# Kernel tuning notes

Measured on AMD Instinct MI355X. Metric: run time of the kernel, lower is better.

## Reference

```python
import jax, jax.numpy as jnp
import numpy as np

D_MODEL = 256
D_INNER = 512   # expand=2
D_STATE = 16
DT_RANK = 16    # ceil(d_model/16)
D_CONV = 4
N_LAYERS = 2    # per direction
B, N = 2, 1024


def _mamba_layer(x, W_in, cw, cb, W_x, W_dt, b_dt, A_log, Dp, W_out):
    """One mamba_ssm.Mamba forward. x: (B, L, d_model)."""
    Bb, L, _ = x.shape
    xz = x @ W_in.T                        # (B, L, 2*d_inner)
    di = xz.shape[-1] // 2
    xc, z = xz[..., :di], xz[..., di:]
    # causal depthwise conv1d, kernel D_CONV, left-pad d_conv-1
    K = cw.shape[-1]
    xp = jnp.pad(xc, ((0, 0), (K - 1, 0), (0, 0)))
    xc = sum(xp[:, k:k + L, :] * cw[:, k] for k in range(K)) + cb
    xc = jax.nn.silu(xc)
    # input-dependent dt, B, C
    dbl = xc @ W_x.T                       # (B, L, dt_rank + 2*d_state)
    ds = A_log.shape[-1]
    dt = dbl[..., :DT_RANK]
    Bm = dbl[..., DT_RANK:DT_RANK + ds]    # (B, L, d_state)
    Cm = dbl[..., DT_RANK + ds:]           # (B, L, d_state)
    dt = jax.nn.softplus(dt @ W_dt.T + b_dt)  # (B, L, d_inner)
    A = -jnp.exp(A_log)                    # (d_inner, d_state)
    dA = jnp.exp(dt[..., None] * A)                          # (B, L, di, ds)
    dBx = dt[..., None] * Bm[:, :, None, :] * xc[..., None]  # (B, L, di, ds)

    def step(h, inp):
        a_t, b_t, c_t = inp                # (B,di,ds),(B,di,ds),(B,ds)
        h = a_t * h + b_t
        y_t = jnp.einsum('bds,bs->bd', h, c_t)
        return h, y_t

    h0 = jnp.zeros((Bb, di, ds), x.dtype)
    _, ys = jax.lax.scan(step, h0, (dA.transpose(1, 0, 2, 3),
                                    dBx.transpose(1, 0, 2, 3),
                                    Cm.transpose(1, 0, 2)))
    y = ys.transpose(1, 0, 2) + xc * Dp    # skip term D*x
    y = y * jax.nn.silu(z)                 # gate
    return y @ W_out.T                     # (B, L, d_model)


def setup_inputs() -> dict:
    key = jax.random.key(0)
    ks = jax.random.split(key, 10)
    s = 0.05  # weight scale for numerical stability
    nlay = 2 * N_LAYERS  # forward layers then backward layers
    return {
        "x": jax.random.normal(ks[0], (B, N, D_MODEL), jnp.float32),
        "in_proj": jax.random.normal(ks[1], (nlay, 2 * D_INNER, D_MODEL), jnp.float32) * s,
        "conv_w": jax.random.normal(ks[2], (nlay, D_INNER, D_CONV), jnp.float32) * s,
        "conv_b": jax.random.normal(ks[3], (nlay, D_INNER), jnp.float32) * s,
        "x_proj": jax.random.normal(ks[4], (nlay, DT_RANK + 2 * D_STATE, D_INNER), jnp.float32) * s,
        "dt_proj": jax.random.normal(ks[5], (nlay, D_INNER, DT_RANK), jnp.float32) * s,
        "dt_bias": jax.random.normal(ks[6], (nlay, D_INNER), jnp.float32) * s,
        "A_log": jax.random.uniform(ks[7], (nlay, D_INNER, D_STATE), jnp.float32),
        "D": jax.random.uniform(ks[8], (nlay, D_INNER), jnp.float32),
        "out_proj": jax.random.normal(ks[9], (nlay, D_MODEL, D_INNER), jnp.float32) * s,
    }


def reference(x, in_proj, conv_w, conv_b, x_proj, dt_proj, dt_bias, A_log, D, out_proj):
    n = in_proj.shape[0] // 2
    x_fwd = x
    for i in range(n):
        x_fwd = _mamba_layer(x_fwd, in_proj[i], conv_w[i], conv_b[i], x_proj[i],
                             dt_proj[i], dt_bias[i], A_log[i], D[i], out_proj[i])
    x_bwd = x[:, ::-1, :]
    for i in range(n, 2 * n):
        x_bwd = _mamba_layer(x_bwd, in_proj[i], conv_w[i], conv_b[i], x_proj[i],
                             dt_proj[i], dt_bias[i], A_log[i], D[i], out_proj[i])
    x_bwd = x_bwd[:, ::-1, :]
    return jnp.concatenate([x_fwd, x_bwd], axis=-1)  # (B, N, 2*d_model)
```

## Files before the change

### kernel.cpp

```cpp
#include <hip/hip_runtime.h>
#include <math.h>

#define G 2
#define BB 2
#define L 1024
#define DM 256
#define DI 512
#define DS 16
#define DR 16
#define CH 64
#define CL 16
#define RTOT (G*BB*L)
#define SKX 8

typedef short bh8 __attribute__((ext_vector_type(8)));
typedef float f4x __attribute__((ext_vector_type(4)));

__device__ __forceinline__ float silu_f(float x) { return x / (1.f + __expf(-x)); }

__device__ __forceinline__ unsigned short f2bf(float f) {
    unsigned u = __float_as_uint(f);
    unsigned r = u + 0x7FFFu + ((u >> 16) & 1u);
    return (unsigned short)(r >> 16);
}
__device__ __forceinline__ float bf2f(unsigned short s) {
    return __uint_as_float(((unsigned)s) << 16);
}

template<int BM, int SPLITK, int AMAP, int CMODE>
__global__ __launch_bounds__(256) void mfma_gemm(
    const float* __restrict__ A, size_t slabOff, int lda, int Ktot,
    const float* __restrict__ W, int Nout, int step,
    float* __restrict__ C, int ldc, size_t partStride)
{
    constexpr int AP = BM / 32;
    constexpr int CA = BM / 32;
    __shared__ short As_hi[BM * 40];
    __shared__ short As_lo[BM * 40];
    __shared__ short Bs_hi[64 * 40];
    __shared__ short Bs_lo[64 * 40];

    const int row0 = blockIdx.y * BM;
    const int col0 = blockIdx.x * 64;
    const int g    = row0 >> 11;
    const int lay  = g * 2 + step;
    const float* Wg = W + (size_t)lay * Nout * Ktot;
    const int t    = threadIdx.x;
    const int lane = t & 63, wv = t >> 6;
    const int m = lane & 15, quad = lane >> 4;
    const int wr = wv >> 1, wc = wv & 1;

    const int Kc    = Ktot / SPLITK;
    const int kbase = blockIdx.z * Kc;
    const int NT    = Kc / 32;

    float4 pa[CA], pa2[CA], pb[2];
    auto loadT = [&](int kt) {
        const int kb = kbase + kt * 32;
        #pragma unroll
        for (int i = 0; i < CA; i++) {
            int id = t + 256 * i;
            int row = id >> 3, kq = id & 7;
            size_t arow;
            if (AMAP == 1) {
                int gr = row0 + row;
                int gg = gr >> 11, b = (gr >> 10) & 1, l = gr & 1023;
                int sl = gg ? (1023 - l) : l;
                arow = (size_t)(b * 1024 + sl);
            } else {
                arow = (size_t)(row0 + row);
            }
            pa[i] = *(const float4*)&A[arow * lda + kb + kq * 4];
            if (AMAP == 2)
                pa2[i] = *(const float4*)&A[slabOff + arow * lda + kb + kq * 4];
        }
        #pragma unroll
        for (int i = 0; i < 2; i++) {
            int id = t + 256 * i;
            int row = id >> 3, kq = id & 7;
            pb[i] = *(const float4*)&Wg[(size_t)(col0 + row) * Ktot + kb + kq * 4];
        }
    };
    auto cvt_store = [&](short* hi, short* lo, int row, int kq, float4 v) {
        short4 h, l;
        unsigned short s;
        s = f2bf(v.x); h.x = (short)s; l.x = (short)f2bf(v.x - bf2f(s));
        s = f2bf(v.y); h.y = (short)s; l.y = (short)f2bf(v.y - bf2f(s));
        s = f2bf(v.z); h.z = (short)s; l.z = (short)f2bf(v.z - bf2f(s));
        s = f2bf(v.w); h.w = (short)s; l.w = (short)f2bf(v.w - bf2f(s));
        *(short4*)&hi[row * 40 + kq * 4] = h;
        *(short4*)&lo[row * 40 + kq * 4] = l;
    };

    f4x acc[AP][2] = {};
    loadT(0);

    for (int kt = 0; kt < NT; kt++) {
        #pragma unroll
        for (int i = 0; i < CA; i++) {
            int id = t + 256 * i;
            int row = id >> 3, kq = id & 7;
            float4 v = pa[i];
            if (AMAP == 2) { v.x += pa2[i].x; v.y += pa2[i].y; v.z += pa2[i].z; v.w += pa2[i].w; }
            cvt_store(As_hi, As_lo, row, kq, v);
        }
        #pragma unroll
        for (int i = 0; i < 2; i++) {
            int id = t + 256 * i;
            int row = id >> 3, kq = id & 7;
            cvt_store(Bs_hi, Bs_lo, row, kq, pb[i]);
        }
        __syncthreads();
        if (kt + 1 < NT) loadT(kt + 1);

        bh8 ah[AP], al[AP], bh[2], bl[2];
        #pragma unroll
        for (int p = 0; p < AP; p++) {
            int r = wr * (BM / 2) + p * 16 + m;
            ah[p] = *(bh8*)&As_hi[r * 40 + quad * 8];
            al[p] = *(bh8*)&As_lo[r * 40 + quad * 8];
        }
        #pragma unroll
        for (int pb_ = 0; pb_ < 2; pb_++) {
            int r = wc * 32 + pb_ * 16 + m;
            bh[pb_] = *(bh8*)&Bs_hi[r * 40 + quad * 8];
            bl[pb_] = *(bh8*)&Bs_lo[r * 40 + quad * 8];
        }
        #pragma unroll
        for (int p = 0; p < AP; p++)
            #pragma unroll
            for (int q = 0; q < 2; q++) {
                acc[p][q] = __builtin_amdgcn_mfma_f32_16x16x32_bf16(ah[p], bh[q], acc[p][q], 0, 0, 0);
                acc[p][q] = __builtin_amdgcn_mfma_f32_16x16x32_bf16(ah[p], bl[q], acc[p][q], 0, 0, 0);
                acc[p][q] = __builtin_amdgcn_mfma_f32_16x16x32_bf16(al[p], bh[q], acc[p][q], 0, 0, 0);
            }
        __syncthreads();
    }

    float* Cz = C + (size_t)blockIdx.z * partStride;
    #pragma unroll
    for (int p = 0; p < AP; p++)
        #pragma unroll
        for (int q = 0; q < 2; q++) {
            int gcol = col0 + wc * 32 + q * 16 + m;
            #pragma unroll
            for (int r = 0; r < 4; r++) {
                int grow = row0 + wr * (BM / 2) + p * 16 + quad * 4 + r;
                if (CMODE == 2) {
                    int b = (grow >> 10) & 1, l = grow & 1023;
                    size_t dst = (g == 0)
                        ? ((size_t)(b * 1024 + l) * 512 + gcol)
                        : ((size_t)(b * 1024 + (1023 - l)) * 512 + 256 + gcol);
                    C[dst] = acc[p][q][r];
                } else {
                    Cz[(size_t)grow * ldc + gcol] = acc[p][q][r];
                }
            }
        }
}

template<int SPLITK>
__global__ __launch_bounds__(256) void gemm_xproj(
    const float* __restrict__ XZ, const float* __restrict__ cw,
    const float* __restrict__ cb, float* __restrict__ XCb,
    const float* __restrict__ W, int step,
    float* __restrict__ C, size_t partStride)
{
    constexpr int Nout = 48, Ktot = DI;
    __shared__ float As[16][68];
    __shared__ float Bs[16][68];

    const int row0 = blockIdx.y * 64;
    const int g    = row0 >> 11;
    const int lay  = g * 2 + step;
    const float* Wg = W + (size_t)lay * Nout * Ktot;
    const int t  = threadIdx.x;
    const int tx = t & 15, ty = t >> 4;
    const int Kc    = Ktot / SPLITK;
    const int kbase = blockIdx.z * Kc;
    const int NT    = Kc / 16;

    const int sr = t >> 2;
    const int sk = (t & 3) * 4;
    const int gr = row0 + sr;
    const int l  = gr & 1023;
    const bool bok = (sr < Nout);

    float4 pa, pb;
    auto loadT = [&](int kt) {
        const int ch = kbase + kt * 16 + sk;
        const float* wb = cw + ((size_t)lay * 512 + ch) * 4;
        float4 w0 = *(const float4*)&wb[0];
        float4 w1 = *(const float4*)&wb[4];
        float4 w2 = *(const float4*)&wb[8];
        float4 w3 = *(const float4*)&wb[12];
        float4 acc = *(const float4*)&cb[(size_t)lay * 512 + ch];
        #pragma unroll
        for (int k = 0; k < 4; k++) {
            if (l - 3 + k < 0) continue;
            float4 xv = *(const float4*)&XZ[(size_t)(gr - 3 + k) * 1024 + ch];
            acc.x += (&w0.x)[k] * xv.x; acc.y += (&w1.x)[k] * xv.y;
            acc.z += (&w2.x)[k] * xv.z; acc.w += (&w3.x)[k] * xv.w;
        }
        acc.x = silu_f(acc.x); acc.y = silu_f(acc.y);
        acc.z = silu_f(acc.z); acc.w = silu_f(acc.w);
        pa = acc;
        *(float4*)&XCb[(size_t)gr * 512 + ch] = acc;
        pb = bok ? *(const float4*)&Wg[(size_t)sr * Ktot + kbase + kt * 16 + sk]
                 : make_float4(0.f, 0.f, 0.f, 0.f);
    };

    float acc[4][4] = {};
    loadT(0);

    for (int kt = 0; kt < NT; kt++) {
        As[sk + 0][sr] = pa.x; As[sk + 1][sr] = pa.y;
        As[sk + 2][sr] = pa.z; As[sk + 3][sr] = pa.w;
        Bs[sk + 0][sr] = pb.x; Bs[sk + 1][sr] = pb.y;
        Bs[sk + 2][sr] = pb.z; Bs[sk + 3][sr] = pb.w;
        __syncthreads();
        if (kt + 1 < NT) loadT(kt + 1);
        #pragma unroll
        for (int kk = 0; kk < 16; kk++) {
            float4 a = *(const float4*)&As[kk][ty * 4];
            float4 b = *(const float4*)&Bs[kk][tx * 4];
            float av[4] = {a.x, a.y, a.z, a.w};
            float bv[4] = {b.x, b.y, b.z, b.w};
            #pragma unroll
            for (int i = 0; i < 4; i++)
                #pragma unroll
                for (int j = 0; j < 4; j++) acc[i][j] += av[i] * bv[j];
        }
        __syncthreads();
    }

    float* Cz = C + (size_t)blockIdx.z * partStride;
    const int col = tx * 4;
    if (col < Nout) {
        #pragma unroll
        for (int i = 0; i < 4; i++) {
            int r = row0 + ty * 4 + i;
            *(float4*)&Cz[(size_t)r * 48 + col] =
                make_float4(acc[i][0], acc[i][1], acc[i][2], acc[i][3]);
        }
    }
}

__device__ __forceinline__ void stage_dbl(
    float dbl[CL][48], const float* __restrict__ Pdbl, int r0, int tid)
{
    for (int id = tid; id < CL * 48; id += 512) {
        int rr = id / 48, cc = id - rr * 48;
        size_t o = (size_t)(r0 + rr) * 48 + cc;
        float v = 0.f;
        #pragma unroll
        for (int s = 0; s < SKX; s++) v += Pdbl[(size_t)s * (RTOT * 48) + o];
        dbl[rr][cc] = v;
    }
}

__global__ __launch_bounds__(512) void scanA(
    const float* __restrict__ XCb, const float* __restrict__ Pdbl,
    const float* __restrict__ A_log, const float* __restrict__ Wdt,
    const float* __restrict__ bdt,
    float* __restrict__ Aprod, float* __restrict__ Hend, int step)
{
    __shared__ float dbl[CL][48];
    int blk = blockIdx.x;
    int c  = blk & (CH - 1);
    int gb = blk >> 6;
    int g  = gb >> 1;
    int lay = g * 2 + step;
    int d = threadIdx.x;
    int r0 = gb * L + c * CL;

    stage_dbl(dbl, Pdbl, r0, threadIdx.x);

    float wdt[16];
    const float* wrow = Wdt + ((size_t)lay * DI + d) * DR;
    #pragma unroll
    for (int k = 0; k < 16; k += 4) {
        float4 v = *(const float4*)&wrow[k];
        wdt[k] = v.x; wdt[k + 1] = v.y; wdt[k + 2] = v.z; wdt[k + 3] = v.w;
    }
    float bias = bdt[(size_t)lay * DI + d];

    float a[DS], h[DS], ap[DS];
    const float* al = A_log + ((size_t)lay * DI + d) * DS;
    #pragma unroll
    for (int s = 0; s < DS; s++) { a[s] = -__expf(al[s]); h[s] = 0.f; ap[s] = 1.f; }
    __syncthreads();

    for (int tt = 0; tt < CL; tt++) {
        float dtr = bias;
        #pragma unroll
        for (int k = 0; k < 16; k++) dtr += dbl[tt][k] * wdt[k];
        float dt = (dtr > 20.f) ? dtr : log1pf(__expf(dtr));
        float xc = XCb[(size_t)(r0 + tt) * DI + d];
        float dx = dt * xc;
        #pragma unroll
        for (int s = 0; s < DS; s++) {
            float da = __expf(dt * a[s]);
            h[s] = da * h[s] + dx * dbl[tt][16 + s];
            ap[s] *= da;
        }
    }
    size_t base = ((size_t)(gb * DI + d) * CH + c) * DS;
    #pragma unroll
    for (int q = 0; q < 4; q++) {
        *(float4*)&Aprod[base + q * 4] = make_float4(ap[q*4], ap[q*4+1], ap[q*4+2], ap[q*4+3]);
        *(float4*)&Hend [base + q * 4] = make_float4(h[q*4],  h[q*4+1],  h[q*4+2],  h[q*4+3]);
    }
}

__global__ __launch_bounds__(256) void scanCombine(
    const float* __restrict__ Aprod, const float* __restrict__ Hend,
    float* __restrict__ Hinit)
{
    int idx = blockIdx.x * 256 + threadIdx.x;
    int s  = idx & 15;
    int gd = idx >> 4;
    size_t base = (size_t)gd * CH * DS + s;
    float h = 0.f;
    for (int c0 = 0; c0 < CH; c0 += 8) {
        float ap[8], e[8];
        #pragma unroll
        for (int j = 0; j < 8; j++) {
            size_t o = base + (size_t)(c0 + j) * DS;
            ap[j] = Aprod[o]; e[j] = Hend[o];
        }
        #pragma unroll
        for (int j = 0; j < 8; j++) {
            Hinit[base + (size_t)(c0 + j) * DS] = h;
            h = ap[j] * h + e[j];
        }
    }
}

__global__ __launch_bounds__(512) void scanB(
    const float* __restrict__ XCb, const float* __restrict__ Pdbl,
    const float* __restrict__ XZ, const float* __restrict__ A_log,
    const float* __restrict__ Wdt, const float* __restrict__ bdt,
    const float* __restrict__ Dp, const float* __restrict__ Hinit,
    float* __restrict__ Yb, int step)
{
    __shared__ float dbl[CL][48];
    int blk = blockIdx.x;
    int c  = blk & (CH - 1);
    int gb = blk >> 6;
    int g  = gb >> 1;
    int lay = g * 2 + step;
    int d = threadIdx.x;
    int r0 = gb * L + c * CL;

    stage_dbl(dbl, Pdbl, r0, threadIdx.x);

    float wdt[16];
    const float* wrow = Wdt + ((size_t)lay * DI + d) * DR;
    #pragma unroll
    for (int k = 0; k < 16; k += 4) {
        float4 v = *(const float4*)&wrow[k];
        wdt[k] = v.x; wdt[k + 1] = v.y; wdt[k + 2] = v.z; wdt[k + 3] = v.w;
    }
    float bias = bdt[(size_t)lay * DI + d];

    float a[DS], h[DS];
    const float* al = A_log + ((size_t)lay * DI + d) * DS;
    size_t base = ((size_t)(gb * DI + d) * CH + c) * DS;
    #pragma unroll
    for (int s = 0; s < DS; s++) { a[s] = -__expf(al[s]); h[s] = Hinit[base + s]; }
    float Dv = Dp[(size_t)lay * DI + d];
    __syncthreads();

    for (int tt = 0; tt < CL; tt++) {
        int r = r0 + tt;
        float dtr = bias;
        #pragma unroll
        for (int k = 0; k < 16; k++) dtr += dbl[tt][k] * wdt[k];
        float dt = (dtr > 20.f) ? dtr : log1pf(__expf(dtr));
        float xc = XCb[(size_t)r * DI + d];
        float dx = dt * xc;
        float y = 0.f;
        #pragma unroll
        for (int s = 0; s < DS; s++) {
            float da = __expf(dt * a[s]);
            h[s] = da * h[s] + dx * dbl[tt][16 + s];
            y += h[s] * dbl[tt][32 + s];
        }
        y += xc * Dv;
        float z = XZ[(size_t)r * 1024 + 512 + d];
        y *= silu_f(z);
        Yb[(size_t)r * DI + d] = y;
    }
}

extern "C" void kernel_launch(void* const* d_in, const int* in_sizes, int n_in,
                              void* d_out, int out_size, void* d_ws, size_t ws_size,
                              hipStream_t stream)
{
    const float* x        = (const float*)d_in[0];
    const float* in_proj  = (const float*)d_in[1];
    const float* conv_w   = (const float*)d_in[2];
    const float* conv_b   = (const float*)d_in[3];
    const float* x_proj   = (const float*)d_in[4];
    const float* dt_proj  = (const float*)d_in[5];
    const float* dt_bias  = (const float*)d_in[6];
    const float* A_log    = (const float*)d_in[7];
    const float* Dp       = (const float*)d_in[8];
    const float* out_proj = (const float*)d_in[9];
    float* out = (float*)d_out;

    float* w = (float*)d_ws;
    size_t o = 0;
    float* XZ    = w + o; o += (size_t)RTOT * 1024;
    float* XCb   = w + o; o += (size_t)RTOT * DI;
    float* Yb    = w + o; o += (size_t)RTOT * DI;
    float* Pdbl  = w + o; o += (size_t)SKX * RTOT * 48;
    float* Aprod = w + o; o += (size_t)G * BB * DI * CH * DS;
    float* Hend  = w + o; o += (size_t)G * BB * DI * CH * DS;
    float* Hinit = w + o; o += (size_t)G * BB * DI * CH * DS;
    float* Pout  = w + o; o += (size_t)2 * RTOT * DM;
    (void)ws_size; (void)in_sizes; (void)n_in; (void)out_size;

    for (int step = 0; step < 2; step++) {
        if (step == 0)
            mfma_gemm<128, 1, 1, 0><<<dim3(16, 32, 1), 256, 0, stream>>>(
                x, 0, DM, DM, in_proj, 2 * DI, 0, XZ, 1024, 0);
        else
            mfma_gemm<128, 1, 2, 0><<<dim3(16, 32, 1), 256, 0, stream>>>(
                Pout, (size_t)RTOT * DM, DM, DM, in_proj, 2 * DI, 1, XZ, 1024, 0);

        gemm_xproj<SKX><<<dim3(1, 64, SKX), 256, 0, stream>>>(
            XZ, conv_w, conv_b, XCb, x_proj, step, Pdbl, (size_t)RTOT * 48);

        scanA<<<G * BB * CH, 512, 0, stream>>>(
            XCb, Pdbl, A_log, dt_proj, dt_bias, Aprod, Hend, step);
        scanCombine<<<(G * BB * DI * DS) / 256, 256, 0, stream>>>(Aprod, Hend, Hinit);
        scanB<<<G * BB * CH, 512, 0, stream>>>(
            XCb, Pdbl, XZ, A_log, dt_proj, dt_bias, Dp, Hinit, Yb, step);

        if (step == 0)
            mfma_gemm<64, 2, 0, 0><<<dim3(4, 64, 2), 256, 0, stream>>>(
                Yb, 0, DI, DI, out_proj, DM, 0, Pout, DM, (size_t)RTOT * DM);
        else
            mfma_gemm<64, 1, 0, 2><<<dim3(4, 64, 1), 256, 0, stream>>>(
                Yb, 0, DI, DI, out_proj, DM, 1, out, DM, 0);
    }
}
```

Measured before the change: 266.3 us.

## Use split-bf16 MFMA for x_proj and cache dt/dbl between scan passes

The fused conv+x_proj GEMM moves from a scalar FP32 outer-product loop to bf16 MFMA with a hi/lo split (three MFMAs per tile) to keep near-FP32 accuracy. scanA now writes the reduced split-K dbl rows and the softplus dt values to workspace. scanB reads these instead of re-reducing the split-K partials and recomputing the dt projection. Both scans preload xc, z and dt into register arrays and fully unroll the time loop, at the cost of extra global traffic for the DTb buffer and more register pressure.

```diff
diff --git a/kernel.cpp b/kernel.cpp
--- a/kernel.cpp
+++ b/kernel.cpp
@@ -160,109 +160,142 @@
 }
 
 template<int SPLITK>
-__global__ __launch_bounds__(256) void gemm_xproj(
+__global__ __launch_bounds__(256) void mfma_xproj(
     const float* __restrict__ XZ, const float* __restrict__ cw,
     const float* __restrict__ cb, float* __restrict__ XCb,
     const float* __restrict__ W, int step,
     float* __restrict__ C, size_t partStride)
 {
     constexpr int Nout = 48, Ktot = DI;
-    __shared__ float As[16][68];
-    __shared__ float Bs[16][68];
+    __shared__ short As_hi[64 * 40];
+    __shared__ short As_lo[64 * 40];
+    __shared__ short Bs_hi[64 * 40];
+    __shared__ short Bs_lo[64 * 40];
 
     const int row0 = blockIdx.y * 64;
     const int g    = row0 >> 11;
     const int lay  = g * 2 + step;
     const float* Wg = W + (size_t)lay * Nout * Ktot;
-    const int t  = threadIdx.x;
-    const int tx = t & 15, ty = t >> 4;
+    const int t    = threadIdx.x;
+    const int lane = t & 63, wv = t >> 6;
+    const int m = lane & 15, quad = lane >> 4;
+    const int wr = wv >> 1, wc = wv & 1;
+
     const int Kc    = Ktot / SPLITK;
     const int kbase = blockIdx.z * Kc;
-    const int NT    = Kc / 16;
-
-    const int sr = t >> 2;
-    const int sk = (t & 3) * 4;
-    const int gr = row0 + sr;
-    const int l  = gr & 1023;
-    const bool bok = (sr < Nout);
-
-    float4 pa, pb;
+    const int NT    = Kc / 32;
+
+    float4 pa[2], pb[2];
     auto loadT = [&](int kt) {
-        const int ch = kbase + kt * 16 + sk;
-        const float* wb = cw + ((size_t)lay * 512 + ch) * 4;
-        float4 w0 = *(const float4*)&wb[0];
-        float4 w1 = *(const float4*)&wb[4];
-        float4 w2 = *(const float4*)&wb[8];
-        float4 w3 = *(const float4*)&wb[12];
-        float4 acc = *(const float4*)&cb[(size_t)lay * 512 + ch];
-        #pragma unroll
-        for (int k = 0; k < 4; k++) {
-            if (l - 3 + k < 0) continue;
-            float4 xv = *(const float4*)&XZ[(size_t)(gr - 3 + k) * 1024 + ch];
-            acc.x += (&w0.x)[k] * xv.x; acc.y += (&w1.x)[k] * xv.y;
-            acc.z += (&w2.x)[k] * xv.z; acc.w += (&w3.x)[k] * xv.w;
-        }
-        acc.x = silu_f(acc.x); acc.y = silu_f(acc.y);
-        acc.z = silu_f(acc.z); acc.w = silu_f(acc.w);
-        pa = acc;
-        *(float4*)&XCb[(size_t)gr * 512 + ch] = acc;
-        pb = bok ? *(const float4*)&Wg[(size_t)sr * Ktot + kbase + kt * 16 + sk]
-                 : make_float4(0.f, 0.f, 0.f, 0.f);
+        const int kb = kbase + kt * 32;
+        #pragma unroll
+        for (int i = 0; i < 2; i++) {
+            int id = t + 256 * i;
+            int row = id >> 3, kq = id & 7;
+            int gr = row0 + row;
+            int l  = gr & 1023;
+            int ch = kb + kq * 4;
+            const float* wb = cw + ((size_t)lay * 512 + ch) * 4;
+            float4 w0 = *(const float4*)&wb[0];
+            float4 w1 = *(const float4*)&wb[4];
+            float4 w2 = *(const float4*)&wb[8];
+            float4 w3 = *(const float4*)&wb[12];
+            float4 acc = *(const float4*)&cb[(size_t)lay * 512 + ch];
+            #pragma unroll
+            for (int k = 0; k < 4; k++) {
+                if (l - 3 + k < 0) continue;
+                float4 xv = *(const float4*)&XZ[(size_t)(gr - 3 + k) * 1024 + ch];
+                acc.x += (&w0.x)[k] * xv.x; acc.y += (&w1.x)[k] * xv.y;
+                acc.z += (&w2.x)[k] * xv.z; acc.w += (&w3.x)[k] * xv.w;
+            }
+            acc.x = silu_f(acc.x); acc.y = silu_f(acc.y);
+            acc.z = silu_f(acc.z); acc.w = silu_f(acc.w);
+            pa[i] = acc;
+            *(float4*)&XCb[(size_t)gr * 512 + ch] = acc;
+        }
+        #pragma unroll
+        for (int i = 0; i < 2; i++) {
+            int id = t + 256 * i;
+            int row = id >> 3, kq = id & 7;
+            pb[i] = (row < Nout)
+                  ? *(const float4*)&Wg[(size_t)row * Ktot + kb + kq * 4]
+                  : make_float4(0.f, 0.f, 0.f, 0.f);
+        }
     };
-
-    float acc[4][4] = {};
+    auto cvt_store = [&](short* hi, short* lo, int row, int kq, float4 v) {
+        short4 h, l;
+        unsigned short s;
+        s = f2bf(v.x); h.x = (short)s; l.x = (short)f2bf(v.x - bf2f(s));
+        s = f2bf(v.y); h.y = (short)s; l.y = (short)f2bf(v.y - bf2f(s));
+        s = f2bf(v.z); h.z = (short)s; l.z = (short)f2bf(v.z - bf2f(s));
+        s = f2bf(v.w); h.w = (short)s; l.w = (short)f2bf(v.w - bf2f(s));
+        *(short4*)&hi[row * 40 + kq * 4] = h;
+        *(short4*)&lo[row * 40 + kq * 4] = l;
+    };
+
+    f4x acc[2][2] = {};
     loadT(0);
 
     for (int kt = 0; kt < NT; kt++) {
-        As[sk + 0][sr] = pa.x; As[sk + 1][sr] = pa.y;
-        As[sk + 2][sr] = pa.z; As[sk + 3][sr] = pa.w;
-        Bs[sk + 0][sr] = pb.x; Bs[sk + 1][sr] = pb.y;
-        Bs[sk + 2][sr] = pb.z; Bs[sk + 3][sr] = pb.w;
+        #pragma unroll
+        for (int i = 0; i < 2; i++) {
+            int id = t + 256 * i;
+            int row = id >> 3, kq = id & 7;
+            cvt_store(As_hi, As_lo, row, kq, pa[i]);
+        }
+        #pragma unroll
+        for (int i = 0; i < 2; i++) {
+            int id = t + 256 * i;
+            int row = id >> 3, kq = id & 7;
+            cvt_store(Bs_hi, Bs_lo, row, kq, pb[i]);
+        }
         __syncthreads();
         if (kt + 1 < NT) loadT(kt + 1);
-        #pragma unroll
-        for (int kk = 0; kk < 16; kk++) {
-            float4 a = *(const float4*)&As[kk][ty * 4];
-            float4 b = *(const float4*)&Bs[kk][tx * 4];
-            float av[4] = {a.x, a.y, a.z, a.w};
-            float bv[4] = {b.x, b.y, b.z, b.w};
+
+        bh8 ah[2], al[2], bh[2], bl[2];
+        #pragma unroll
+        for (int p = 0; p < 2; p++) {
+            int r = wr * 32 + p * 16 + m;
+            ah[p] = *(bh8*)&As_hi[r * 40 + quad * 8];
+            al[p] = *(bh8*)&As_lo[r * 40 + quad * 8];
+        }
+        #pragma unroll
+        for (int q = 0; q < 2; q++) {
+            int r = wc * 32 + q * 16 + m;
+            bh[q] = *(bh8*)&Bs_hi[r * 40 + quad * 8];
+            bl[q] = *(bh8*)&Bs_lo[r * 40 + quad * 8];
+        }
+        #pragma unroll
+        for (int p = 0; p < 2; p++)
             #pragma unroll
-            for (int i = 0; i < 4; i++)
-                #pragma unroll
-                for (int j = 0; j < 4; j++) acc[i][j] += av[i] * bv[j];
-        }
+            for (int q = 0; q < 2; q++) {
+                acc[p][q] = __builtin_amdgcn_mfma_f32_16x16x32_bf16(ah[p], bh[q], acc[p][q], 0, 0, 0);
+                acc[p][q] = __builtin_amdgcn_mfma_f32_16x16x32_bf16(ah[p], bl[q], acc[p][q], 0, 0, 0);
+                acc[p][q] = __builtin_amdgcn_mfma_f32_16x16x32_bf16(al[p], bh[q], acc[p][q], 0, 0, 0);
+            }
         __syncthreads();
     }
 
     float* Cz = C + (size_t)blockIdx.z * partStride;
-    const int col = tx * 4;
-    if (col < Nout) {
-        #pragma unroll
-        for (int i = 0; i < 4; i++) {
-            int r = row0 + ty * 4 + i;
-            *(float4*)&Cz[(size_t)r * 48 + col] =
-                make_float4(acc[i][0], acc[i][1], acc[i][2], acc[i][3]);
-        }
-    }
-}
-
-__device__ __forceinline__ void stage_dbl(
-    float dbl[CL][48], const float* __restrict__ Pdbl, int r0, int tid)
-{
-    for (int id = tid; id < CL * 48; id += 512) {
-        int rr = id / 48, cc = id - rr * 48;
-        size_t o = (size_t)(r0 + rr) * 48 + cc;
-        float v = 0.f;
-        #pragma unroll
-        for (int s = 0; s < SKX; s++) v += Pdbl[(size_t)s * (RTOT * 48) + o];
-        dbl[rr][cc] = v;
-    }
+    #pragma unroll
+    for (int p = 0; p < 2; p++)
+        #pragma unroll
+        for (int q = 0; q < 2; q++) {
+            int gcol = wc * 32 + q * 16 + m;
+            if (gcol >= Nout) continue;
+            #pragma unroll
+            for (int r = 0; r < 4; r++) {
+                int grow = row0 + wr * 32 + p * 16 + quad * 4 + r;
+                Cz[(size_t)grow * 48 + gcol] = acc[p][q][r];
+            }
+        }
 }
 
 __global__ __launch_bounds__(512) void scanA(
     const float* __restrict__ XCb, const float* __restrict__ Pdbl,
     const float* __restrict__ A_log, const float* __restrict__ Wdt,
     const float* __restrict__ bdt,
+    float* __restrict__ DBLc, float* __restrict__ DTb,
     float* __restrict__ Aprod, float* __restrict__ Hend, int step)
 {
     __shared__ float dbl[CL][48];
@@ -274,7 +307,15 @@
     int d = threadIdx.x;
     int r0 = gb * L + c * CL;
 
-    stage_dbl(dbl, Pdbl, r0, threadIdx.x);
+    for (int id = threadIdx.x; id < CL * 48; id += 512) {
+        int rr = id / 48, cc = id - rr * 48;
+        size_t o = (size_t)(r0 + rr) * 48 + cc;
+        float v = 0.f;
+        #pragma unroll
+        for (int s = 0; s < SKX; s++) v += Pdbl[(size_t)s * (RTOT * 48) + o];
+        dbl[rr][cc] = v;
+        DBLc[o] = v;
+    }
 
     float wdt[16];
     const float* wrow = Wdt + ((size_t)lay * DI + d) * DR;
@@ -285,19 +326,24 @@
     }
     float bias = bdt[(size_t)lay * DI + d];
 
+    float xc[CL];
+    #pragma unroll
+    for (int tt = 0; tt < CL; tt++) xc[tt] = XCb[(size_t)(r0 + tt) * DI + d];
+
     float a[DS], h[DS], ap[DS];
     const float* al = A_log + ((size_t)lay * DI + d) * DS;
     #pragma unroll
     for (int s = 0; s < DS; s++) { a[s] = -__expf(al[s]); h[s] = 0.f; ap[s] = 1.f; }
     __syncthreads();
 
+    #pragma unroll
     for (int tt = 0; tt < CL; tt++) {
         float dtr = bias;
         #pragma unroll
         for (int k = 0; k < 16; k++) dtr += dbl[tt][k] * wdt[k];
         float dt = (dtr > 20.f) ? dtr : log1pf(__expf(dtr));
-        float xc = XCb[(size_t)(r0 + tt) * DI + d];
-        float dx = dt * xc;
+        DTb[(size_t)(r0 + tt) * DI + d] = dt;
+        float dx = dt * xc[tt];
         #pragma unroll
         for (int s = 0; s < DS; s++) {
             float da = __expf(dt * a[s]);
@@ -338,11 +384,10 @@
 }
 
 __global__ __launch_bounds__(512) void scanB(
-    const float* __restrict__ XCb, const float* __restrict__ Pdbl,
+    const float* __restrict__ XCb, const float* __restrict__ DBLc,
     const float* __restrict__ XZ, const float* __restrict__ A_log,
-    const float* __restrict__ Wdt, const float* __restrict__ bdt,
-    const float* __restrict__ Dp, const float* __restrict__ Hinit,
-    float* __restrict__ Yb, int step)
+    const float* __restrict__ DTb, const float* __restrict__ Dp,
+    const float* __restrict__ Hinit, float* __restrict__ Yb, int step)
 {
     __shared__ float dbl[CL][48];
     int blk = blockIdx.x;
@@ -353,16 +398,18 @@
     int d = threadIdx.x;
     int r0 = gb * L + c * CL;
 
-    stage_dbl(dbl, Pdbl, r0, threadIdx.x);
-
-    float wdt[16];
-    const float* wrow = Wdt + ((size_t)lay * DI + d) * DR;
-    #pragma unroll
-    for (int k = 0; k < 16; k += 4) {
-        float4 v = *(const float4*)&wrow[k];
-        wdt[k] = v.x; wdt[k + 1] = v.y; wdt[k + 2] = v.z; wdt[k + 3] = v.w;
-    }
-    float bias = bdt[(size_t)lay * DI + d];
+    for (int id = threadIdx.x; id < CL * 48; id += 512) {
+        int rr = id / 48, cc = id - rr * 48;
+        dbl[rr][cc] = DBLc[(size_t)(r0 + rr) * 48 + cc];
+    }
+
+    float xc[CL], zz[CL], dt[CL];
+    #pragma unroll
+    for (int tt = 0; tt < CL; tt++) xc[tt] = XCb[(size_t)(r0 + tt) * DI + d];
+    #pragma unroll
+    for (int tt = 0; tt < CL; tt++) zz[tt] = XZ[(size_t)(r0 + tt) * 1024 + 512 + d];
+    #pragma unroll
+    for (int tt = 0; tt < CL; tt++) dt[tt] = DTb[(size_t)(r0 + tt) * DI + d];
 
     float a[DS], h[DS];
     const float* al = A_log + ((size_t)lay * DI + d) * DS;
@@ -372,25 +419,19 @@
     float Dv = Dp[(size_t)lay * DI + d];
     __syncthreads();
 
+    #pragma unroll
     for (int tt = 0; tt < CL; tt++) {
-        int r = r0 + tt;
-        float dtr = bias;
-        #pragma unroll
-        for (int k = 0; k < 16; k++) dtr += dbl[tt][k] * wdt[k];
-        float dt = (dtr > 20.f) ? dtr : log1pf(__expf(dtr));
-        float xc = XCb[(size_t)r * DI + d];
-        float dx = dt * xc;
+        float dx = dt[tt] * xc[tt];
         float y = 0.f;
         #pragma unroll
         for (int s = 0; s < DS; s++) {
-            float da = __expf(dt * a[s]);
+            float da = __expf(dt[tt] * a[s]);
             h[s] = da * h[s] + dx * dbl[tt][16 + s];
             y += h[s] * dbl[tt][32 + s];
         }
-        y += xc * Dv;
-        float z = XZ[(size_t)r * 1024 + 512 + d];
-        y *= silu_f(z);
-        Yb[(size_t)r * DI + d] = y;
+        y += xc[tt] * Dv;
+        y *= silu_f(zz[tt]);
+        Yb[(size_t)(r0 + tt) * DI + d] = y;
     }
 }
 
@@ -416,6 +457,8 @@
     float* XCb   = w + o; o += (size_t)RTOT * DI;
     float* Yb    = w + o; o += (size_t)RTOT * DI;
     float* Pdbl  = w + o; o += (size_t)SKX * RTOT * 48;
+    float* DBLc  = w + o; o += (size_t)RTOT * 48;
+    float* DTb   = w + o; o += (size_t)RTOT * DI;
     float* Aprod = w + o; o += (size_t)G * BB * DI * CH * DS;
     float* Hend  = w + o; o += (size_t)G * BB * DI * CH * DS;
     float* Hinit = w + o; o += (size_t)G * BB * DI * CH * DS;
@@ -430,14 +473,14 @@
             mfma_gemm<128, 1, 2, 0><<<dim3(16, 32, 1), 256, 0, stream>>>(
                 Pout, (size_t)RTOT * DM, DM, DM, in_proj, 2 * DI, 1, XZ, 1024, 0);
 
-        gemm_xproj<SKX><<<dim3(1, 64, SKX), 256, 0, stream>>>(
+        mfma_xproj<SKX><<<dim3(1, 64, SKX), 256, 0, stream>>>(
             XZ, conv_w, conv_b, XCb, x_proj, step, Pdbl, (size_t)RTOT * 48);
 
         scanA<<<G * BB * CH, 512, 0, stream>>>(
-            XCb, Pdbl, A_log, dt_proj, dt_bias, Aprod, Hend, step);
+            XCb, Pdbl, A_log, dt_proj, dt_bias, DBLc, DTb, Aprod, Hend, step);
         scanCombine<<<(G * BB * DI * DS) / 256, 256, 0, stream>>>(Aprod, Hend, Hinit);
         scanB<<<G * BB * CH, 512, 0, stream>>>(
-            XCb, Pdbl, XZ, A_log, dt_proj, dt_bias, Dp, Hinit, Yb, step);
+            XCb, DBLc, XZ, A_log, DTb, Dp, Hinit, Yb, step);
 
         if (step == 0)
             mfma_gemm<64, 2, 0, 0><<<dim3(4, 64, 2), 256, 0, stream>>>(
```

New measurement: 280.0 us. 1.05x slower.

## Fuse out_proj GEMM into scan phase-B kernel via LDS-staged bf16x3 MFMA

Applied to the files above, without the earlier changes.

The scanB kernel now keeps its gated output for a 16-row chunk in shared memory as hi/lo bf16 pairs, then multiplies it by out_proj with MFMA and writes the projected result straight to Pout or to the final output. This drops the Yb intermediate, the separate out_proj GEMM launch and the split-K partial buffer, so the next in_proj no longer sums two slabs. In exchange, each of the 256 blocks reloads and converts the whole 256x512 out_proj weight from global memory with no reuse across blocks, and the M tile is only 16 rows, which adds a lot of redundant weight traffic and conversion ALU work.

```diff
diff --git a/kernel.cpp b/kernel.cpp
--- a/kernel.cpp
+++ b/kernel.cpp
@@ -12,6 +12,7 @@
 #define CL 16
 #define RTOT (G*BB*L)
 #define SKX 8
+#define YSTR 520
 
 typedef short bh8 __attribute__((ext_vector_type(8)));
 typedef float f4x __attribute__((ext_vector_type(4)));
@@ -27,9 +28,9 @@
     return __uint_as_float(((unsigned)s) << 16);
 }
 
-template<int BM, int SPLITK, int AMAP, int CMODE>
+template<int BM, int SPLITK, int AMAP>
 __global__ __launch_bounds__(256) void mfma_gemm(
-    const float* __restrict__ A, size_t slabOff, int lda, int Ktot,
+    const float* __restrict__ A, int lda, int Ktot,
     const float* __restrict__ W, int Nout, int step,
     float* __restrict__ C, int ldc, size_t partStride)
 {
@@ -54,7 +55,7 @@
     const int kbase = blockIdx.z * Kc;
     const int NT    = Kc / 32;
 
-    float4 pa[CA], pa2[CA], pb[2];
+    float4 pa[CA], pb[2];
     auto loadT = [&](int kt) {
         const int kb = kbase + kt * 32;
         #pragma unroll
@@ -71,8 +72,6 @@
                 arow = (size_t)(row0 + row);
             }
             pa[i] = *(const float4*)&A[arow * lda + kb + kq * 4];
-            if (AMAP == 2)
-                pa2[i] = *(const float4*)&A[slabOff + arow * lda + kb + kq * 4];
         }
         #pragma unroll
         for (int i = 0; i < 2; i++) {
@@ -100,9 +99,7 @@
         for (int i = 0; i < CA; i++) {
             int id = t + 256 * i;
             int row = id >> 3, kq = id & 7;
-            float4 v = pa[i];
-            if (AMAP == 2) { v.x += pa2[i].x; v.y += pa2[i].y; v.z += pa2[i].z; v.w += pa2[i].w; }
-            cvt_store(As_hi, As_lo, row, kq, v);
+            cvt_store(As_hi, As_lo, row, kq, pa[i]);
         }
         #pragma unroll
         for (int i = 0; i < 2; i++) {
@@ -146,15 +143,7 @@
             #pragma unroll
             for (int r = 0; r < 4; r++) {
                 int grow = row0 + wr * (BM / 2) + p * 16 + quad * 4 + r;
-                if (CMODE == 2) {
-                    int b = (grow >> 10) & 1, l = grow & 1023;
-                    size_t dst = (g == 0)
-                        ? ((size_t)(b * 1024 + l) * 512 + gcol)
-                        : ((size_t)(b * 1024 + (1023 - l)) * 512 + 256 + gcol);
-                    C[dst] = acc[p][q][r];
-                } else {
-                    Cz[(size_t)grow * ldc + gcol] = acc[p][q][r];
-                }
+                Cz[(size_t)grow * ldc + gcol] = acc[p][q][r];
             }
         }
 }
@@ -337,14 +326,17 @@
     }
 }
 
-__global__ __launch_bounds__(512) void scanB(
+template<int OUTMODE>
+__global__ __launch_bounds__(512) void scanB_fused(
     const float* __restrict__ XCb, const float* __restrict__ Pdbl,
     const float* __restrict__ XZ, const float* __restrict__ A_log,
     const float* __restrict__ Wdt, const float* __restrict__ bdt,
     const float* __restrict__ Dp, const float* __restrict__ Hinit,
-    float* __restrict__ Yb, int step)
+    const float* __restrict__ Wout, float* __restrict__ Cout, int step)
 {
     __shared__ float dbl[CL][48];
+    __shared__ short Ys_hi[CL * YSTR];
+    __shared__ short Ys_lo[CL * YSTR];
     int blk = blockIdx.x;
     int c  = blk & (CH - 1);
     int gb = blk >> 6;
@@ -390,7 +382,56 @@
         y += xc * Dv;
         float z = XZ[(size_t)r * 1024 + 512 + d];
         y *= silu_f(z);
-        Yb[(size_t)r * DI + d] = y;
+        unsigned short hs = f2bf(y);
+        Ys_hi[tt * YSTR + d] = (short)hs;
+        Ys_lo[tt * YSTR + d] = (short)f2bf(y - bf2f(hs));
+    }
+    __syncthreads();
+
+    const int lane = threadIdx.x & 63, wv = threadIdx.x >> 6;
+    const int m = lane & 15, quad = lane >> 4;
+    const float* Wg2 = Wout + (size_t)lay * DM * DI;
+
+    #pragma unroll
+    for (int q = 0; q < 2; q++) {
+        const int coln = wv * 32 + q * 16 + m;
+        const float* wp = Wg2 + (size_t)coln * DI;
+        f4x acc = {};
+        #pragma unroll
+        for (int k0 = 0; k0 < DI; k0 += 32) {
+            const int kk = k0 + quad * 8;
+            float4 w0 = *(const float4*)&wp[kk];
+            float4 w1 = *(const float4*)&wp[kk + 4];
+            bh8 bhv, blv;
+            {
+                float vv[8] = {w0.x, w0.y, w0.z, w0.w, w1.x, w1.y, w1.z, w1.w};
+                #pragma unroll
+                for (int j = 0; j < 8; j++) {
+                    unsigned short hsj = f2bf(vv[j]);
+                    bhv[j] = (short)hsj;
+                    blv[j] = (short)f2bf(vv[j] - bf2f(hsj));
+                }
+            }
+            bh8 ahv = *(bh8*)&Ys_hi[m * YSTR + kk];
+            bh8 alv = *(bh8*)&Ys_lo[m * YSTR + kk];
+            acc = __builtin_amdgcn_mfma_f32_16x16x32_bf16(ahv, bhv, acc, 0, 0, 0);
+            acc = __builtin_amdgcn_mfma_f32_16x16x32_bf16(ahv, blv, acc, 0, 0, 0);
+            acc = __builtin_amdgcn_mfma_f32_16x16x32_bf16(alv, bhv, acc, 0, 0, 0);
+        }
+        #pragma unroll
+        for (int r = 0; r < 4; r++) {
+            int tt = quad * 4 + r;
+            int grow = r0 + tt;
+            if (OUTMODE == 0) {
+                Cout[(size_t)grow * DM + coln] = acc[r];
+            } else {
+                int b = (grow >> 10) & 1, l = grow & 1023;
+                size_t dst = (g == 0)
+                    ? ((size_t)(b * 1024 + l) * 512 + coln)
+                    : ((size_t)(b * 1024 + (1023 - l)) * 512 + 256 + coln);
+                Cout[dst] = acc[r];
+            }
+        }
     }
 }
 
@@ -414,21 +455,20 @@
     size_t o = 0;
     float* XZ    = w + o; o += (size_t)RTOT * 1024;
     float* XCb   = w + o; o += (size_t)RTOT * DI;
-    float* Yb    = w + o; o += (size_t)RTOT * DI;
     float* Pdbl  = w + o; o += (size_t)SKX * RTOT * 48;
     float* Aprod = w + o; o += (size_t)G * BB * DI * CH * DS;
     float* Hend  = w + o; o += (size_t)G * BB * DI * CH * DS;
     float* Hinit = w + o; o += (size_t)G * BB * DI * CH * DS;
-    float* Pout  = w + o; o += (size_t)2 * RTOT * DM;
+    float* Pout  = w + o; o += (size_t)RTOT * DM;
     (void)ws_size; (void)in_sizes; (void)n_in; (void)out_size;
 
     for (int step = 0; step < 2; step++) {
         if (step == 0)
-            mfma_gemm<128, 1, 1, 0><<<dim3(16, 32, 1), 256, 0, stream>>>(
-                x, 0, DM, DM, in_proj, 2 * DI, 0, XZ, 1024, 0);
+            mfma_gemm<128, 1, 1><<<dim3(16, 32, 1), 256, 0, stream>>>(
+                x, DM, DM, in_proj, 2 * DI, 0, XZ, 1024, 0);
         else
-            mfma_gemm<128, 1, 2, 0><<<dim3(16, 32, 1), 256, 0, stream>>>(
-                Pout, (size_t)RTOT * DM, DM, DM, in_proj, 2 * DI, 1, XZ, 1024, 0);
+            mfma_gemm<128, 1, 0><<<dim3(16, 32, 1), 256, 0, stream>>>(
+                Pout, DM, DM, in_proj, 2 * DI, 1, XZ, 1024, 0);
 
         gemm_xproj<SKX><<<dim3(1, 64, SKX), 256, 0, stream>>>(
             XZ, conv_w, conv_b, XCb, x_proj, step, Pdbl, (size_t)RTOT * 48);
@@ -436,14 +476,13 @@
         scanA<<<G * BB * CH, 512, 0, stream>>>(
             XCb, Pdbl, A_log, dt_proj, dt_bias, Aprod, Hend, step);
         scanCombine<<<(G * BB * DI * DS) / 256, 256, 0, stream>>>(Aprod, Hend, Hinit);
-        scanB<<<G * BB * CH, 512, 0, stream>>>(
-            XCb, Pdbl, XZ, A_log, dt_proj, dt_bias, Dp, Hinit, Yb, step);
-
         if (step == 0)
-            mfma_gemm<64, 2, 0, 0><<<dim3(4, 64, 2), 256, 0, stream>>>(
-                Yb, 0, DI, DI, out_proj, DM, 0, Pout, DM, (size_t)RTOT * DM);
+            scanB_fused<0><<<G * BB * CH, 512, 0, stream>>>(
+                XCb, Pdbl, XZ, A_log, dt_proj, dt_bias, Dp, Hinit,
+                out_proj, Pout, 0);
         else
-            mfma_gemm<64, 1, 0, 2><<<dim3(4, 64, 1), 256, 0, stream>>>(
-                Yb, 0, DI, DI, out_proj, DM, 1, out, DM, 0);
-    }
-}
+            scanB_fused<1><<<G * BB * CH, 512, 0, stream>>>(
+                XCb, Pdbl, XZ, A_log, dt_proj, dt_bias, Dp, Hinit,
+                out_proj, out, 1);
+    }
+}
```

New measurement: 263.4 us. No clear change (-1.1%).
